# Optimization experiments

Hardware: AMD Instinct MI355X
Metric: run time of the kernel (lower is better)

The kernel has to match this reference:

```python
import jax, jax.numpy as jnp
import numpy as np

B = 2048
NUM_ITER = 3  # dynamic routing iterations


def _conv2d(x, w, b, pad):
    # x: [B,C,H,W], w: [O,I,kh,kw] (OIHW)
    y = jax.lax.conv_general_dilated(
        x, w, window_strides=(1, 1), padding=[(pad, pad), (pad, pad)],
        dimension_numbers=('NCHW', 'OIHW', 'NCHW'))
    return y + b[None, :, None, None]


def _maxpool2(x):
    return jax.lax.reduce_window(x, -jnp.inf, jax.lax.max,
                                 (1, 1, 2, 2), (1, 1, 2, 2), 'VALID')


def _squash(t, axis=-1):
    # scale = |t|^2/(1+|t|^2); out = scale * t / |t|
    n2 = jnp.sum(t * t, axis=axis, keepdims=True)
    return (n2 / (1.0 + n2)) * t * jax.lax.rsqrt(n2)


def setup_inputs() -> dict:
    key = jax.random.key(0)
    ks = jax.random.split(key, 8)
    f32 = jnp.float32
    rn = lambda k, s, sc=1.0: jax.random.normal(k, s, f32) * sc
    return {
        'x': rn(ks[0], (B, 1, 36, 60)),
        'y': rn(ks[1], (B, 2)),
        'conv1_w': rn(ks[2], (20, 1, 5, 5), 0.1),
        'conv1_b': jnp.zeros((20,), f32),
        'conv2_w': rn(ks[3], (50, 20, 5, 5), 0.01),
        'conv2_b': jnp.zeros((50,), f32),
        'pcaps_w': rn(ks[4], (16, 50, 5, 5), 0.05),   # 4 capsules x 4 out-ch, stacked
        'pcaps_b': jnp.zeros((16,), f32),
        'route_w': rn(ks[5], (2, 288, 4, 1)),          # [num_caps, route_nodes, in_ch, out_ch]
        'fc1_w': rn(ks[6], (500, 3602), 0.02),
        'fc1_b': jnp.zeros((500,), f32),
        'fc2_w': rn(ks[7], (2, 502), 0.05),
        'fc2_b': jnp.zeros((2,), f32),
    }


def reference(x, y, conv1_w, conv1_b, conv2_w, conv2_b, pcaps_w, pcaps_b,
              route_w, fc1_w, fc1_b, fc2_w, fc2_b):
    b = x.shape[0]
    # conv backbone
    h = _maxpool2(_conv2d(x, conv1_w, conv1_b, 0))   # [B,20,16,28]
    h = _maxpool2(_conv2d(h, conv2_w, conv2_b, 0))   # [B,50,6,12]

    # primary capsules: 4 parallel convs (stacked into one), each [B,4,6,12]
    p = _conv2d(h, pcaps_w, pcaps_b, 2)              # [B,16,6,12]
    u = p.reshape(b, 4, 4 * 6 * 12)                  # [B, caps=4, nodes=288] (c,h,w flatten per capsule)
    u = u.transpose(0, 2, 1)                         # [B,288,4]
    u = _squash(u, axis=-1)

    # digit capsules: dynamic routing
    # priors[k,b,r,o] = sum_c u[b,r,c] * W[k,r,c,o]
    priors = jnp.einsum('brc,krco->kbro', u, route_w)  # [2,B,288,1]
    logits = jnp.zeros_like(priors)
    v = None
    for i in range(NUM_ITER):
        probs = jax.nn.softmax(logits, axis=2)
        v = _squash(jnp.sum(probs * priors, axis=2, keepdims=True), axis=-1)  # [2,B,1,1]
        if i < NUM_ITER - 1:
            logits = logits + jnp.sum(priors * v, axis=-1, keepdims=True)

    c = v[:, :, 0, :].transpose(1, 0, 2).reshape(b, -1)  # [B,2]
    xf = h.reshape(b, -1)                                # [B,3600]
    f = jnp.concatenate([xf, c], axis=-1)                # [B,3602]
    f = jax.nn.relu(f @ fc1_w.T + fc1_b)                 # [B,500]
    f = jnp.concatenate([f, y], axis=1)                  # [B,502]
    return f @ fc2_w.T + fc2_b                           # [B,2]
```

## Files before the change

### kernel.cpp

```cpp
#include <hip/hip_runtime.h>
#include <math.h>


#define BATCH 2048
#define KP 3712

typedef __attribute__((ext_vector_type(8))) short short8;
typedef __attribute__((ext_vector_type(4))) float floatx4;
typedef unsigned short u16;
typedef unsigned int   u32;

#define GLD(gp, lp) __builtin_amdgcn_global_load_lds( \
    (const __attribute__((address_space(1))) u32*)(gp), \
    (__attribute__((address_space(3))) u32*)(lp), 16, 0, 0)

__device__ inline float wave_sum(float v) {
#pragma unroll
    for (int off = 32; off >= 1; off >>= 1) v += __shfl_xor(v, off);
    return v;
}
__device__ inline float wave_max(float v) {
#pragma unroll
    for (int off = 32; off >= 1; off >>= 1) v = fmaxf(v, __shfl_xor(v, off));
    return v;
}
__device__ inline u16 f2bf(float f) {
    u32 u = __float_as_uint(f);
    u32 r = (u + 0x7FFFu + ((u >> 16) & 1u)) >> 16;
    return (u16)r;
}

__global__ __launch_bounds__(256) void k_prep(
    const float* __restrict__ fw,  u16* __restrict__ w_bf,
    const float* __restrict__ w2,  u16* __restrict__ w2t,
    const float* __restrict__ pcw, u16* __restrict__ w_pc,
    const float* __restrict__ w1,  u16* __restrict__ w1t,
    const float* __restrict__ f1b, const float* __restrict__ f2w,
    float* __restrict__ wtab)
{
    __shared__ __align__(16) float srow[3600];
    const int blk = blockIdx.x, t = threadIdx.x;
    if (blk < 500) {
        const int n = blk;
        const float* src = fw + (size_t)n * 3602;
        for (int i = t; i < 1800; i += 256)
            *(float2*)&srow[2 * i] = *(const float2*)&src[2 * i];
        __syncthreads();
        u32* dst = (u32*)(w_bf + (size_t)n * KP);
        for (int i = t; i < 1856; i += 256) {
            int k2 = 2 * i;
            u32 pk = 0u;
            if (k2 < 3600) {
                int pos = k2 / 50, oc = k2 - 50 * pos;
                pk = (u32)f2bf(srow[oc * 72 + pos])
                   | ((u32)f2bf(srow[(oc + 1) * 72 + pos]) << 16);
            }
            dst[i] = pk;
        }
    } else if (blk == 500) {
        u32* z = (u32*)(w_bf + (size_t)500 * KP);
        for (int i = t; i < 22272; i += 256) z[i] = 0u;
    } else if (blk < 526) {
        int g   = (blk - 501) * 256 + t;
        int idx = g * 8;
        int tap = idx >> 11;
        int oc  = (idx >> 5) & 63;
        int ic0 = idx & 31;
        u16 v[8];
#pragma unroll
        for (int j = 0; j < 8; ++j) {
            int ic = ic0 + j;
            float f = (ic < 20 && oc < 50) ? w2[oc * 500 + ic * 25 + tap] : 0.f;
            v[j] = f2bf(f);
        }
        *(short8*)&w2t[idx] = *(short8*)v;
    } else if (blk < 539) {
        int g = (blk - 526) * 256 + t;
        if (g >= 3200) return;
        int idx = g * 8;
        int tap = idx >> 10;
        int rem = idx & 1023;
        int oc  = rem >> 6;
        int ic0 = rem & 63;
        u16 v[8];
#pragma unroll
        for (int j = 0; j < 8; ++j) {
            int ic = ic0 + j;
            float f = (ic < 50) ? pcw[(oc * 50 + ic) * 25 + tap] : 0.f;
            v[j] = f2bf(f);
        }
        *(short8*)&w_pc[idx] = *(short8*)v;
    } else if (blk == 539) {
        if (t < 128) {
            int n  = t >> 2;
            int k0 = (t & 3) * 8;
            u16 v[8];
#pragma unroll
            for (int j = 0; j < 8; ++j) {
                int k = k0 + j;
                float f = (n < 20 && k < 25) ? w1[n * 25 + k] : 0.f;
                v[j] = f2bf(f);
            }
            *(short8*)&w1t[t * 8] = *(short8*)v;
        }
    } else {
        for (int nn = t; nn < 512; nn += 256) {
            float bias = 0.f, wc0 = 0.f, wc1 = 0.f, f20 = 0.f, f21 = 0.f;
            if (nn < 500) {
                bias = f1b[nn];
                wc0  = fw[(size_t)nn * 3602 + 3600];
                wc1  = fw[(size_t)nn * 3602 + 3601];
                f20  = f2w[nn];
                f21  = f2w[502 + nn];
            }
            *(float4*)&wtab[nn * 8]     = make_float4(bias, wc0, wc1, f20);
            *(float4*)&wtab[nn * 8 + 4] = make_float4(f21, 0.f, 0.f, 0.f);
        }
    }
}

__global__ __launch_bounds__(256, 3) void k_convs(
    const float* __restrict__ x, const u16* __restrict__ w1t,
    const float* __restrict__ b1, const u16* __restrict__ w2t,
    const float* __restrict__ b2, const u16* __restrict__ w_pc,
    const float* __restrict__ pcb, const float* __restrict__ rw,
    u32* __restrict__ h_bf, float* __restrict__ cbuf)
{
    __shared__ __align__(16) u16 smem[24704];
    u16* h1t = smem;
    u16* xbf = smem + 17920;
    u16* im2 = smem + 20224;

    const int t = threadIdx.x;
    const int b = blockIdx.x;

    for (int i = t; i < 2688; i += 256) {
        int pos = i / 6, c = i - 6 * pos;
        ((u32*)h1t)[pos * 20 + 10 + c] = 0u;
    }
    const float* xb = x + b * 2160;
    for (int i = t; i < 2160; i += 256) {
        int r = i / 60, c = i - 60 * r;
        xbf[r * 64 + c] = f2bf(xb[i]);
    }
    __syncthreads();

    const int lane = t & 63, w = t >> 6;
    const int r16  = lane & 15;
    const int q    = lane >> 4;

    short8 w1f[2];
#pragma unroll
    for (int nt = 0; nt < 2; ++nt)
        w1f[nt] = *(const short8*)&w1t[(nt * 16 + r16) * 32 + q * 8];

    const int p_   = t;
    const int px_  = p_ >> 2;
    const int dy_  = (p_ & 3) >> 1, dx_ = p_ & 1;
    const int xc_  = 2 * px_ + dx_;
    const int j0_  = xc_ >> 1;
    const int par_ = xc_ & 1;
    const int sw_  = (p_ >> 3) & 3;

#pragma unroll 1
    for (int c = 0; c < 16; ++c) {
        if (t < 112) {
            u16 tap[25];
#pragma unroll
            for (int r = 0; r < 5; ++r) {
                const u32* U = (const u32*)&xbf[(2 * c + dy_ + r) * 64];
                u32 A0 = U[j0_], A1 = U[j0_ + 1], A2 = U[j0_ + 2];
                u16 e0 = par_ ? (u16)(A0 >> 16) : (u16)A0;
                u16 e1 = par_ ? (u16)A1         : (u16)(A0 >> 16);
                u16 e2 = par_ ? (u16)(A1 >> 16) : (u16)A1;
                u16 e3 = par_ ? (u16)A2         : (u16)(A1 >> 16);
                u16 e4 = par_ ? (u16)(A2 >> 16) : (u16)A2;
                tap[r * 5 + 0] = e0; tap[r * 5 + 1] = e1; tap[r * 5 + 2] = e2;
                tap[r * 5 + 3] = e3; tap[r * 5 + 4] = e4;
            }
            u32 ow[16];
#pragma unroll
            for (int j = 0; j < 12; ++j)
                ow[j] = (u32)tap[2 * j] | ((u32)tap[2 * j + 1] << 16);
            ow[12] = (u32)tap[24];
            ow[13] = 0u; ow[14] = 0u; ow[15] = 0u;
            u32* dst = (u32*)&im2[p_ * 40];
            *(uint4*)&dst[(0 ^ sw_) * 4] = make_uint4(ow[0],  ow[1],  ow[2],  ow[3]);
            *(uint4*)&dst[(1 ^ sw_) * 4] = make_uint4(ow[4],  ow[5],  ow[6],  ow[7]);
            *(uint4*)&dst[(2 ^ sw_) * 4] = make_uint4(ow[8],  ow[9],  ow[10], ow[11]);
            *(uint4*)&dst[(3 ^ sw_) * 4] = make_uint4(ow[12], ow[13], ow[14], ow[15]);
        }
        __syncthreads();
#pragma unroll
        for (int mi = 0; mi < 2; ++mi) {
            int mt = w + 4 * mi;
            if (mt < 7) {
                int m  = mt * 16 + r16;
                int sr = (m >> 3) & 3;
                short8 af = *(const short8*)&im2[m * 40 + ((q ^ sr) * 8)];
                floatx4 a1[2] = {};
#pragma unroll
                for (int nt = 0; nt < 2; ++nt)
                    a1[nt] = __builtin_amdgcn_mfma_f32_16x16x32_bf16(
                        af, w1f[nt], a1[nt], 0, 0, 0);
                int pq = mt * 4 + q;
#pragma unroll
                for (int nt = 0; nt < 2; ++nt) {
                    int oc = nt * 16 + r16;
                    if (oc < 20) {
                        floatx4 a = a1[nt];
                        float v = fmaxf(fmaxf(a[0], a[1]), fmaxf(a[2], a[3]))
                                + b1[oc];
                        h1t[(c * 28 + pq) * 40 + oc] = f2bf(v);
                    }
                }
            }
        }
        __syncthreads();
    }

    int abase[5];
#pragma unroll
    for (int i = 0; i < 5; ++i) {
        int mt = w + 4 * i;
        if (mt < 18) {
            int m  = mt * 16 + r16;
            int pq = m >> 2, sub = m & 3;
            int py = pq / 12, px = pq - py * 12;
            int yy = py * 2 + (sub >> 1);
            int xx = px * 2 + (sub & 1);
            abase[i] = (yy * 28 + xx) * 40 + q * 8;
        } else abase[i] = 0;
    }
    floatx4 acc2[5][4] = {};
    const u16* wtb = w2t + r16 * 32 + q * 8;

    short8 bf[4];
#pragma unroll
    for (int nt = 0; nt < 4; ++nt)
        bf[nt] = *(const short8*)&wtb[nt * 512];

#pragma unroll 1
    for (int tap = 0; tap < 25; ++tap) {
        short8 bfn[4];
        if (tap < 24) {
#pragma unroll
            for (int nt = 0; nt < 4; ++nt)
                bfn[nt] = *(const short8*)&wtb[(tap + 1) * 2048 + nt * 512];
        }
        int r = tap / 5, s = tap - 5 * r;
        int aoff = r * 1120 + s * 40;
#pragma unroll
        for (int i = 0; i < 5; ++i) {
            int mt = w + 4 * i;
            if (mt < 18) {
                short8 af = *(const short8*)&h1t[abase[i] + aoff];
#pragma unroll
                for (int nt = 0; nt < 4; ++nt)
                    acc2[i][nt] = __builtin_amdgcn_mfma_f32_16x16x32_bf16(
                        af, bf[nt], acc2[i][nt], 0, 0, 0);
            }
        }
#pragma unroll
        for (int nt = 0; nt < 4; ++nt) bf[nt] = bfn[nt];
    }
    __syncthreads();

    float* hs2 = (float*)smem;
#pragma unroll
    for (int i = 0; i < 5; ++i) {
        int mt = w + 4 * i;
        if (mt < 18) {
            int pq = mt * 4 + q;
#pragma unroll
            for (int nt = 0; nt < 4; ++nt) {
                int oc = nt * 16 + r16;
                if (oc < 50) {
                    floatx4 a = acc2[i][nt];
                    hs2[pq * 50 + oc] =
                        fmaxf(fmaxf(a[0], a[1]), fmaxf(a[2], a[3])) + b2[oc];
                }
            }
        }
    }
    for (int i = t; i < 6336; i += 256)
        ((u32*)smem)[3600 + i] = 0u;
    __syncthreads();

    u16* hsbuf = smem + 7200;
    u32* ho = h_bf + (size_t)b * 1856;
    for (int i = t; i < 1856; i += 256) {
        if (i < 1800) {
            int k2 = 2 * i;
            u32 pk = (u32)f2bf(hs2[k2]) | ((u32)f2bf(hs2[k2 + 1]) << 16);
            ho[i] = pk;
            int pos = k2 / 50;
            int oc  = k2 - 50 * pos;
            int ph  = pos / 12, pw = pos - 12 * ph;
            ((u32*)hsbuf)[((((ph + 2) * 16) + pw + 2) * 72 + oc) >> 1] = pk;
        } else ho[i] = 0u;
    }
    __syncthreads();

    int pbase[5];
#pragma unroll
    for (int mt = 0; mt < 5; ++mt) {
        int m  = mt * 16 + r16;
        int ph = m / 12, pw = m - 12 * ph;
        pbase[mt] = (ph * 16 + pw) * 72 + q * 8;
    }
    floatx4 pacc[5] = {};
    const u16* wp = w_pc + r16 * 64 + q * 8;
    const int ntap = (28 - w) >> 2;
#pragma unroll 1
    for (int tt = 0; tt < ntap; ++tt) {
        int tap = w + 4 * tt;
        short8 b0 = *(const short8*)&wp[tap * 1024];
        short8 b1 = *(const short8*)&wp[tap * 1024 + 32];
        int r = tap / 5, s = tap - 5 * r;
        int aoff = (r * 16 + s) * 72;
#pragma unroll
        for (int mt = 0; mt < 5; ++mt) {
            short8 a0 = *(const short8*)&hsbuf[pbase[mt] + aoff];
            short8 a1 = *(const short8*)&hsbuf[pbase[mt] + aoff + 32];
            pacc[mt] = __builtin_amdgcn_mfma_f32_16x16x32_bf16(a0, b0, pacc[mt], 0, 0, 0);
            pacc[mt] = __builtin_amdgcn_mfma_f32_16x16x32_bf16(a1, b1, pacc[mt], 0, 0, 0);
        }
    }
    __syncthreads();

    float* psum = (float*)(smem + 7200);
#pragma unroll
    for (int mt = 0; mt < 5; ++mt)
#pragma unroll
        for (int i = 0; i < 4; ++i) {
            int m = mt * 16 + q * 4 + i;
            psum[w * 1360 + m * 17 + r16] = pacc[mt][i];
        }
    __syncthreads();

    for (int i = t; i < 1152; i += 256) {
        int m = i >> 4, oc = i & 15;
        int a = m * 17 + oc;
        float s = psum[a] + psum[1360 + a] + psum[2720 + a] + psum[4080 + a]
                + pcb[oc];
        psum[a] = s;
    }
    __syncthreads();

    float* pri = (float*)(smem + 19872);
    for (int r = t; r < 288; r += 256) {
        int sub = r / 72;
        int pos = r - sub * 72;
        float u0 = psum[pos * 17 + 0  + sub];
        float u1 = psum[pos * 17 + 4  + sub];
        float u2 = psum[pos * 17 + 8  + sub];
        float u3 = psum[pos * 17 + 12 + sub];
        float n2 = u0 * u0 + u1 * u1 + u2 * u2 + u3 * u3;
        float scale = (n2 / (1.0f + n2)) * rsqrtf(n2);
        u0 *= scale; u1 *= scale; u2 *= scale; u3 *= scale;
#pragma unroll
        for (int k = 0; k < 2; ++k) {
            const float4 wv = *(const float4*)&rw[(k * 288 + r) * 4];
            pri[k * 288 + r] = u0 * wv.x + u1 * wv.y + u2 * wv.z + u3 * wv.w;
        }
    }
    __syncthreads();

    if (w < 2) {
        const float* pr = &pri[w * 288];
        float p[5];
        bool  val[5];
#pragma unroll
        for (int j = 0; j < 5; ++j) {
            int r  = j * 64 + lane;
            val[j] = r < 288;
            p[j]   = val[j] ? pr[r] : 0.0f;
        }
        float tot = wave_sum(p[0] + p[1] + p[2] + p[3] + p[4]);
        float s = tot * (1.0f / 288.0f);
        float a = s * fabsf(s) / (1.0f + s * s);
#pragma unroll
        for (int it = 0; it < 2; ++it) {
            float l[5];
            float lm = -INFINITY;
#pragma unroll
            for (int j = 0; j < 5; ++j) {
                l[j] = val[j] ? p[j] * a : -INFINITY;
                lm   = fmaxf(lm, l[j]);
            }
            lm = wave_max(lm);
            float se = 0.f, sp = 0.f;
#pragma unroll
            for (int j = 0; j < 5; ++j) {
                float e = val[j] ? expf(l[j] - lm) : 0.f;
                se += e;
                sp += e * p[j];
            }
            se = wave_sum(se);
            sp = wave_sum(sp);
            float sv = sp / se;
            float v  = sv * fabsf(sv) / (1.0f + sv * sv);
            if (it == 0) a += v;
            else if (lane == 0) cbuf[b * 2 + w] = v;
        }
    }
}

__global__ __launch_bounds__(256) void k_fc1(
    const u16* __restrict__ h_bf, const u16* __restrict__ w_bf,
    float* __restrict__ f1buf)
{
    __shared__ __align__(16) u16 As[64 * 32];
    __shared__ __align__(16) u16 Bs[64 * 32];
    const int t = threadIdx.x;
    const int lane = t & 63, w = t >> 6;
    const int m0 = blockIdx.x * 64;
    const int n0 = blockIdx.y * 64;
    const int s  = blockIdx.z;
    const int k0 = s * 928;

    const u16* ga = h_bf + (size_t)(m0 + (t >> 2)) * KP + k0 + (t & 3) * 8;
    const u16* gb = w_bf + (size_t)(n0 + (t >> 2)) * KP + k0 + (t & 3) * 8;
    u16* lA = As + w * 512;
    u16* lB = Bs + w * 512;

    const int r16 = lane & 15, q = lane >> 4;
    const int ar = (w * 16 + r16) * 32 + q * 8;
    const int br = r16 * 32 + q * 8;

    floatx4 acc[4] = {};
#pragma unroll 1
    for (int it = 0; it < 29; ++it) {
        const int ko = it * 32;
        GLD(ga + ko, lA);
        GLD(gb + ko, lB);
        __syncthreads();
        short8 af = *(const short8*)&As[ar];
#pragma unroll
        for (int nt = 0; nt < 4; ++nt) {
            short8 bfv = *(const short8*)&Bs[br + nt * 512];
            acc[nt] = __builtin_amdgcn_mfma_f32_16x16x32_bf16(af, bfv, acc[nt], 0, 0, 0);
        }
        __syncthreads();
    }

    float* fo = f1buf + (size_t)s * (2048 * 512);
    const int mb = m0 + w * 16;
#pragma unroll
    for (int nt = 0; nt < 4; ++nt) {
        int n = n0 + nt * 16 + r16;
#pragma unroll
        for (int i = 0; i < 4; ++i) {
            int m = mb + q * 4 + i;
            fo[(size_t)m * 512 + n] = acc[nt][i];
        }
    }
}

__global__ __launch_bounds__(256) void k_fc2(
    const float* __restrict__ f1buf, const float* __restrict__ wtab,
    const float* __restrict__ cc, const float* __restrict__ y,
    const float* __restrict__ f2w, const float* __restrict__ f2b,
    float* __restrict__ out)
{
    const int b = blockIdx.x * 4 + (threadIdx.x >> 6);
    const int lane = threadIdx.x & 63;
    const float* fb = f1buf + (size_t)b * 512;
    const float c0 = cc[b * 2], c1 = cc[b * 2 + 1];
    float s0 = 0.f, s1 = 0.f;
#pragma unroll
    for (int j = 0; j < 8; ++j) {
        int n = lane + j * 64;
        float raw = fb[n] + fb[1048576 + n] + fb[2097152 + n] + fb[3145728 + n];
        float4 t0 = *(const float4*)&wtab[n * 8];
        float  f21 = wtab[n * 8 + 4];
        float v = fmaxf(raw + t0.x + c0 * t0.y + c1 * t0.z, 0.f);
        s0 += v * t0.w;
        s1 += v * f21;
    }
    s0 = wave_sum(s0);
    s1 = wave_sum(s1);
    if (lane == 0) {
        float y0 = y[b * 2], y1 = y[b * 2 + 1];
        out[b * 2]     = s0 + f2b[0] + y0 * f2w[500] + y1 * f2w[501];
        out[b * 2 + 1] = s1 + f2b[1] + y0 * f2w[1002] + y1 * f2w[1003];
    }
}

extern "C" void kernel_launch(void* const* d_in, const int* in_sizes, int n_in,
                              void* d_out, int out_size, void* d_ws, size_t ws_size,
                              hipStream_t stream) {
    const float* x    = (const float*)d_in[0];
    const float* y    = (const float*)d_in[1];
    const float* c1w  = (const float*)d_in[2];
    const float* c1b  = (const float*)d_in[3];
    const float* c2w  = (const float*)d_in[4];
    const float* c2b  = (const float*)d_in[5];
    const float* pcw  = (const float*)d_in[6];
    const float* pcb  = (const float*)d_in[7];
    const float* rw   = (const float*)d_in[8];
    const float* f1w  = (const float*)d_in[9];
    const float* f1b  = (const float*)d_in[10];
    const float* f2w  = (const float*)d_in[11];
    const float* f2b  = (const float*)d_in[12];
    float* out = (float*)d_out;

    u32*   h_bf  = (u32*)d_ws;
    u16*   w_bf  = (u16*)(h_bf + (size_t)BATCH * 1856);
    u16*   w2t   = w_bf + (size_t)512 * KP;
    u16*   w_pc  = w2t + 51200;
    u16*   w1t   = w_pc + 25600;
    float* cbuf  = (float*)(w1t + 1024);
    float* wtab  = cbuf + 4096;
    float* f1buf = wtab + 4096;

    k_prep<<<541, 256, 0, stream>>>(f1w, w_bf, c2w, w2t, pcw, w_pc, c1w, w1t,
                                    f1b, f2w, wtab);
    k_convs<<<BATCH, 256, 0, stream>>>(x, w1t, c1b, w2t, c2b, w_pc, pcb, rw,
                                       h_bf, cbuf);
    dim3 g4(32, 8, 4);
    k_fc1<<<g4, 256, 0, stream>>>((const u16*)h_bf, w_bf, f1buf);
    k_fc2<<<BATCH / 4, 256, 0, stream>>>(f1buf, wtab, cbuf, y, f2w, f2b, out);
}
```

Before: 236.5 us.

## Split fused conv kernel into conv1 and conv2+primary-caps kernels via global buffer

Splits the fused convolution kernel into two launches. The first runs conv1 and its pooling with a smaller LDS footprint and a higher occupancy target, then writes the pooled activations to global memory. The second reloads them into the padded LDS layout and runs conv2, the primary capsules and routing. This targets better occupancy for each stage, but adds a global write and read of about 36 MB, plus an extra launch. The intermediate buffer reuses the f1buf workspace region, which risks overrunning the workspace if that region is too small.

```diff
diff --git a/kernel.cpp b/kernel.cpp
--- a/kernel.cpp
+++ b/kernel.cpp
@@ -119,25 +119,18 @@
     }
 }
 
-__global__ __launch_bounds__(256, 3) void k_convs(
+__global__ __launch_bounds__(256, 4) void k_conv1(
     const float* __restrict__ x, const u16* __restrict__ w1t,
-    const float* __restrict__ b1, const u16* __restrict__ w2t,
-    const float* __restrict__ b2, const u16* __restrict__ w_pc,
-    const float* __restrict__ pcb, const float* __restrict__ rw,
-    u32* __restrict__ h_bf, float* __restrict__ cbuf)
+    const float* __restrict__ b1, u32* __restrict__ h1g)
 {
-    __shared__ __align__(16) u16 smem[24704];
-    u16* h1t = smem;
-    u16* xbf = smem + 17920;
-    u16* im2 = smem + 20224;
+    __shared__ __align__(16) u16 smem[15744];
+    u16* xbf = smem;
+    u16* im2 = smem + 2304;
+    u16* h1s = smem + 6784;
 
     const int t = threadIdx.x;
     const int b = blockIdx.x;
 
-    for (int i = t; i < 2688; i += 256) {
-        int pos = i / 6, c = i - 6 * pos;
-        ((u32*)h1t)[pos * 20 + 10 + c] = 0u;
-    }
     const float* xb = x + b * 2160;
     for (int i = t; i < 2160; i += 256) {
         int r = i / 60, c = i - 60 * r;
@@ -211,13 +204,48 @@
                         floatx4 a = a1[nt];
                         float v = fmaxf(fmaxf(a[0], a[1]), fmaxf(a[2], a[3]))
                                 + b1[oc];
-                        h1t[(c * 28 + pq) * 40 + oc] = f2bf(v);
+                        h1s[(c * 28 + pq) * 20 + oc] = f2bf(v);
                     }
                 }
             }
         }
         __syncthreads();
     }
+
+    u32* hg = h1g + (size_t)b * 4480;
+    for (int i = t; i < 4480; i += 256) hg[i] = ((u32*)h1s)[i];
+}
+
+__global__ __launch_bounds__(256, 3) void k_conv2p(
+    const u32* __restrict__ h1g, const u16* __restrict__ w2t,
+    const float* __restrict__ b2, const u16* __restrict__ w_pc,
+    const float* __restrict__ pcb, const float* __restrict__ rw,
+    u32* __restrict__ h_bf, float* __restrict__ cbuf)
+{
+    __shared__ __align__(16) u16 smem[24704];
+    u16* h1t = smem;
+
+    const int t = threadIdx.x;
+    const int b = blockIdx.x;
+
+    for (int i = t; i < 2688; i += 256) {
+        int pos = i / 6, c = i - 6 * pos;
+        ((u32*)h1t)[pos * 20 + 10 + c] = 0u;
+    }
+    {
+        const u32* hg = h1g + (size_t)b * 4480;
+        for (int i = t; i < 4480; i += 256) {
+            u32 v = hg[i];
+            int e = 2 * i;
+            int row = e / 20, c0 = e - 20 * row;
+            ((u32*)h1t)[row * 20 + (c0 >> 1)] = v;
+        }
+    }
+    __syncthreads();
+
+    const int lane = t & 63, w = t >> 6;
+    const int r16  = lane & 15;
+    const int q    = lane >> 4;
 
     int abase[5];
 #pragma unroll
@@ -514,11 +542,13 @@
     float* cbuf  = (float*)(w1t + 1024);
     float* wtab  = cbuf + 4096;
     float* f1buf = wtab + 4096;
+    u32*   h1g   = (u32*)f1buf;
 
     k_prep<<<541, 256, 0, stream>>>(f1w, w_bf, c2w, w2t, pcw, w_pc, c1w, w1t,
                                     f1b, f2w, wtab);
-    k_convs<<<BATCH, 256, 0, stream>>>(x, w1t, c1b, w2t, c2b, w_pc, pcb, rw,
-                                       h_bf, cbuf);
+    k_conv1<<<BATCH, 256, 0, stream>>>(x, w1t, c1b, h1g);
+    k_conv2p<<<BATCH, 256, 0, stream>>>(h1g, w2t, c2b, w_pc, pcb, rw,
+                                        h_bf, cbuf);
     dim3 g4(32, 8, 4);
     k_fc1<<<g4, 256, 0, stream>>>((const u16*)h_bf, w_bf, f1buf);
     k_fc2<<<BATCH / 4, 256, 0, stream>>>(f1buf, wtab, cbuf, y, f2w, f2b, out);
```

Measured after the change: 242.5 us. +2.6%, slower.
